# Kernel tuning notes

Hardware: AMD Instinct MI355X
Metric: run time of the kernel (lower is better)

## Reference

```python
import jax, jax.numpy as jnp
import numpy as np

B_MOL = 512      # molecules in batch
A_PER = 64       # atoms per molecule (uniform -> scopes are regular)
EU_PER = 2 * A_PER   # undirected bonds per molecule (ring + skip ring)
ED_PER = 2 * EU_PER  # directed bonds per molecule
N_ATOMS = B_MOL * A_PER
N_DIR = B_MOL * ED_PER
AF, BF = 98, 111
H, HEADS, DEPTH, MLP = 256, 8, 10, 512
DK = H // HEADS
ATOM_OUT, BOND_OUT = 128, 32


def _graph_indices():
    ar = np.arange(A_PER)
    su = np.concatenate([ar, ar])
    du = np.concatenate([(ar + 1) % A_PER, (ar + 2) % A_PER])
    src = np.concatenate([su, du])   # directed: fwd then rev copies
    dst = np.concatenate([du, su])
    rev = np.concatenate([np.arange(EU_PER) + EU_PER, np.arange(EU_PER)])
    offa = (np.arange(B_MOL) * A_PER)[:, None]
    offb = (np.arange(B_MOL) * ED_PER)[:, None]
    b2a = (src[None] + offa).reshape(-1).astype(np.int32)
    b2t = (dst[None] + offa).reshape(-1).astype(np.int32)
    b2rev = (rev[None] + offb).reshape(-1).astype(np.int32)
    pairs = np.stack([(su[None] + offa).reshape(-1), (du[None] + offa).reshape(-1)], 1).astype(np.int32)
    return jnp.asarray(b2a), jnp.asarray(b2t), jnp.asarray(b2rev), jnp.asarray(pairs)


def setup_inputs() -> dict:
    key = jax.random.key(0)
    ks = jax.random.split(key, 24)
    g = lambda k, s: jax.random.normal(k, s, jnp.float32) / np.sqrt(s[0])
    b2a, b2t, b2rev, bond_pairs = _graph_indices()
    return {
        'f_atoms': jax.random.normal(ks[0], (N_ATOMS, AF), jnp.float32),
        'f_bonds': jax.random.normal(ks[1], (N_DIR, BF), jnp.float32),
        'prev_hid': jnp.zeros((N_ATOMS, H), jnp.float32),
        'b2a': b2a, 'b2t': b2t, 'b2rev': b2rev, 'bond_pairs': bond_pairs,
        'W_i': g(ks[2], (BF, H)), 'W_h': g(ks[3], (H, H)),
        'W_o': g(ks[4], (AF + H, H)), 'b_o': jnp.zeros((H,), jnp.float32),
        'Wq': g(ks[5], (H, H)), 'Wk': g(ks[6], (H, H)),
        'Wv': g(ks[7], (H, H)), 'Wattn': g(ks[8], (H, H)),
        'W_vv': jnp.eye(H, dtype=jnp.float32), 'W_vc': g(ks[9], (H, H)),
        'A1': g(ks[10], (H, MLP)), 'a1': jnp.zeros((MLP,), jnp.float32),
        'A2': g(ks[11], (MLP, ATOM_OUT)), 'a2': jnp.zeros((ATOM_OUT,), jnp.float32),
        'B1': g(ks[12], (2 * H, MLP)), 'b1': jnp.zeros((MLP,), jnp.float32),
        'B2': g(ks[13], (MLP, BOND_OUT)), 'b2b': jnp.zeros((BOND_OUT,), jnp.float32),
        'G1': g(ks[14], (H, MLP)), 'g1': jnp.zeros((MLP,), jnp.float32),
        'G2': g(ks[15], (MLP, 1)), 'g2': jnp.zeros((1,), jnp.float32),
    }


def reference(f_atoms, f_bonds, prev_hid, b2a, b2t, b2rev, bond_pairs,
              W_i, W_h, W_o, b_o, Wq, Wk, Wv, Wattn, W_vv, W_vc,
              A1, a1, A2, a2, B1, b1, B2, b2b, G1, g1, G2, g2):
    # ---- DMPNN encoder (directed bond messages) ----
    h0 = jax.nn.relu(f_bonds @ W_i)                     # [E_dir, H]
    h = h0
    for _ in range(DEPTH - 1):
        a_sum = jax.ops.segment_sum(h, b2t, num_segments=N_ATOMS)  # incoming msg per atom
        m = a_sum[b2a] - h[b2rev]                       # exclude reverse bond
        h = jax.nn.relu(h0 + m @ W_h)
    a_in = jax.ops.segment_sum(h, b2t, num_segments=N_ATOMS)
    a_feats = jax.nn.relu(jnp.concatenate([f_atoms, a_in], 1) @ W_o + b_o)  # [N, H]

    # ---- Global_Attention over per-molecule scopes (uniform sizes -> reshape) ----
    x = a_feats.reshape(B_MOL, A_PER, H)
    q = (x @ Wq).reshape(B_MOL, A_PER, HEADS, DK)
    k = (x @ Wk).reshape(B_MOL, A_PER, HEADS, DK)
    v = (x @ Wv).reshape(B_MOL, A_PER, HEADS, DK)
    scores = jnp.einsum('bqhd,bkhd->bhqk', q, k) / np.sqrt(DK)
    attn = jax.nn.softmax(scores, axis=-1)
    ctx = jnp.einsum('bhqk,bkhd->bqhd', attn, v).reshape(B_MOL, A_PER, H)
    a_feats = (x + ctx @ Wattn).reshape(N_ATOMS, H)     # residual MHA

    # ---- recurrent atom state update ----
    atom_feats = jax.nn.relu(prev_hid @ W_vv.T + a_feats @ W_vc.T)  # [N, H]

    # ---- gather-based readout heads ----
    bond_feats = jnp.concatenate([atom_feats[bond_pairs[:, 0]],
                                  atom_feats[bond_pairs[:, 1]]], axis=1)  # [E_und, 2H]
    graph_vecs = atom_feats.reshape(B_MOL, A_PER, H).sum(axis=1)          # [B, H]

    atom_outs = jax.nn.relu(atom_feats @ A1 + a1) @ A2 + a2   # [N, ATOM_OUT]
    bond_outs = jax.nn.relu(bond_feats @ B1 + b1) @ B2 + b2b  # [E_und, BOND_OUT]
    graph_outs = jax.nn.relu(graph_vecs @ G1 + g1) @ G2 + g2  # [B, 1]

    # per-molecule edit scores: [bond scores | atom scores | graph score]
    edit_scores = jnp.concatenate([bond_outs.reshape(B_MOL, -1),
                                   atom_outs.reshape(B_MOL, -1),
                                   graph_outs], axis=1)
    return edit_scores
```

## Files before the change

kernel.cpp:

```cpp
#include <hip/hip_runtime.h>
#include <cstdint>
#include <cstddef>

#define B_MOL 512
#define A_PER 64
#define ED_PER 256
#define N_ATOMS (B_MOL * A_PER)
#define N_DIR (B_MOL * ED_PER)
#define N_UND (B_MOL * 128)
#define HID 256
#define OUT_STRIDE 12289
#define AP 40
#define CP 72

typedef __attribute__((ext_vector_type(8))) short bf16x8;
typedef __attribute__((ext_vector_type(8))) unsigned short u16x8;
typedef __attribute__((ext_vector_type(4))) float f32x4;

#define MFMA(a, b, c) __builtin_amdgcn_mfma_f32_16x16x32_bf16(a, b, c, 0, 0, 0)

__device__ __forceinline__ float b2f(unsigned short s) {
  return __builtin_bit_cast(float, (unsigned)s << 16);
}
__device__ __forceinline__ void split2(float v, unsigned short& h, unsigned short& l) {
  unsigned ub = __builtin_bit_cast(unsigned, v);
  h = (unsigned short)(ub >> 16);
  float fh = __builtin_bit_cast(float, ub & 0xffff0000u);
  float r = v - fh;
  l = (unsigned short)(__builtin_bit_cast(unsigned, r) >> 16);
}
__device__ __forceinline__ int e_src(int e) {
  return (e < 64) ? e : (e < 128) ? (e - 64)
       : (e < 192) ? ((e - 127) & 63) : ((e - 190) & 63);
}

__global__ __launch_bounds__(256) void convAll(
    const float* Wi, const float* Wh, const float* Wo,
    const float* Wq, const float* Wk, const float* Wv,
    const float* Wattn, const float* Wvc, const float* Wvv,
    const float* A1, const float* A2, const float* B1, const float* B2,
    unsigned short* WiTh, unsigned short* WiTl,
    unsigned short* WhTh, unsigned short* WhTl,
    unsigned short* WoTh, unsigned short* WoTl,
    unsigned short* WqkvTh, unsigned short* WqkvTl,
    unsigned short* WaTh, unsigned short* WaTl,
    unsigned short* WcvTh, unsigned short* WcvTl,
    unsigned short* A1Th, unsigned short* A1Tl,
    unsigned short* A2Th, unsigned short* A2Tl,
    unsigned short* B1Th, unsigned short* B1Tl,
    unsigned short* B2Th, unsigned short* B2Tl) {
  int b = blockIdx.x;
  const float *src = nullptr, *src2 = nullptr;
  unsigned short *dh = nullptr, *dl = nullptr;
  int K = 256, N = 256, Kp = 256, mode = 0, n = 0;
  if (b < 2048) {
    int seg = b >> 8; n = b & 255;
    switch (seg) {
      case 0: src = Wi; dh = WiTh; dl = WiTl; K = 111; Kp = 128; break;
      case 1: src = Wh; dh = WhTh; dl = WhTl; break;
      case 2: src = Wo; dh = WoTh; dl = WoTl; K = 354; Kp = 384; mode = 1; break;
      case 3: src = Wq; dh = WqkvTh; dl = WqkvTl; break;
      case 4: src = Wk; dh = WqkvTh + 65536; dl = WqkvTl + 65536; break;
      case 5: src = Wv; dh = WqkvTh + 131072; dl = WqkvTl + 131072; break;
      case 6: src = Wattn; dh = WaTh; dl = WaTl; break;
      default: src = Wvc; src2 = Wvv; dh = WcvTh; dl = WcvTl; K = 512; Kp = 512; mode = 2; break;
    }
  } else if (b < 2560) { n = b - 2048; src = A1; dh = A1Th; dl = A1Tl; K = 256; N = 512; Kp = 256; }
  else if (b < 2688)   { n = b - 2560; src = A2; dh = A2Th; dl = A2Tl; K = 512; N = 128; Kp = 512; }
  else if (b < 3200)   { n = b - 2688; src = B1; dh = B1Th; dl = B1Tl; K = 512; N = 512; Kp = 512; }
  else                 { n = b - 3200; src = B2; dh = B2Th; dl = B2Tl; K = 512; N = 32;  Kp = 512; }
  for (int k = threadIdx.x; k < Kp; k += 256) {
    float v = 0.f;
    if (mode == 0) { if (k < K) v = src[(size_t)k * N + n]; }
    else if (mode == 1) {
      if (k < 256) v = src[(size_t)(98 + k) * 256 + n];
      else if (k < 354) v = src[(size_t)(k - 256) * 256 + n];
    } else {
      v = (k < 256) ? src[(size_t)n * 256 + k] : src2[(size_t)n * 256 + (k - 256)];
    }
    unsigned short h_, l_;
    split2(v, h_, l_);
    dh[(size_t)n * Kp + k] = h_;
    dl[(size_t)n * Kp + k] = l_;
  }
}

template <int AMODE>
__launch_bounds__(256, 3)
__global__ void mgemm(const void* Aa_, const void* Ab_, const void* Ac_, const void* Ad_,
                      const unsigned short* __restrict__ BTh,
                      const unsigned short* __restrict__ BTl, int ldb,
                      const unsigned short* addH, const unsigned short* addL,
                      const float* __restrict__ bias,
                      const float* __restrict__ abias,
                      void* outA, void* outB,
                      int M, int N, int K, int lda, int ldco, int outcol,
                      int relu, int outmode) {
  __shared__ unsigned short AsH[128 * AP], AsL[128 * AP];
  __shared__ unsigned short BsH[128 * AP], BsL[128 * AP];
  const int tid = threadIdx.x;
  const int lane = tid & 63;
  const int l15 = lane & 15, l4 = lane >> 4;
  const int w = tid >> 6;
  const int wr = (w >> 1) * 64, wc = (w & 1) * 64;
  const int tileM = blockIdx.x * 128, tileN = blockIdx.y * 128;
  const int srow = tid >> 1;
  const int sks = (tid & 1) * 16;

  int rem = N - tileN - wc;
  int bnMax = rem >= 64 ? 4 : (rem > 0 ? (rem >> 4) : 0);

  f32x4 zf = {0.f, 0.f, 0.f, 0.f};
  f32x4 acc[4][4];
#pragma unroll
  for (int i = 0; i < 4; ++i)
#pragma unroll
    for (int j = 0; j < 4; ++j) acc[i][j] = zf;

  const int nkb = (K + 31) >> 5;
  for (int kb = 0; kb < nkb; ++kb) {
    __syncthreads();
    const int k0 = kb * 32 + sks;
    {
      const int row = tileM + srow;
      if (AMODE == 1 || (AMODE == 3 && k0 < 256)) {
        const unsigned short* Ah = (const unsigned short*)Aa_;
        const unsigned short* Al = (const unsigned short*)Ab_;
        size_t bse = (AMODE == 3) ? ((size_t)row * 256 + k0)
                                  : ((size_t)row * lda + k0);
        *(u16x8*)&AsH[srow * AP + sks]     = *(const u16x8*)&Ah[bse];
        *(u16x8*)&AsH[srow * AP + sks + 8] = *(const u16x8*)&Ah[bse + 8];
        *(u16x8*)&AsL[srow * AP + sks]     = *(const u16x8*)&Al[bse];
        *(u16x8*)&AsL[srow * AP + sks + 8] = *(const u16x8*)&Al[bse + 8];
      } else if (AMODE == 5) {
        int mol = row >> 7, u = row & 127;
        int a0 = (u < 64) ? u : (u - 64);
        int a1v = (u < 64) ? ((u + 1) & 63) : ((u - 62) & 63);
        size_t p1 = (size_t)(mol * 64 + a0) * 512 + k0;
        size_t p2 = (size_t)(mol * 64 + a1v) * 512 + k0;
        const unsigned short* P1h = (const unsigned short*)Aa_;
        const unsigned short* P1l = (const unsigned short*)Ab_;
        const unsigned short* P2h = (const unsigned short*)Ac_;
        const unsigned short* P2l = (const unsigned short*)Ad_;
        u16x8 x1h[2] = {*(const u16x8*)&P1h[p1], *(const u16x8*)&P1h[p1 + 8]};
        u16x8 x1l[2] = {*(const u16x8*)&P1l[p1], *(const u16x8*)&P1l[p1 + 8]};
        u16x8 x2h[2] = {*(const u16x8*)&P2h[p2], *(const u16x8*)&P2h[p2 + 8]};
        u16x8 x2l[2] = {*(const u16x8*)&P2l[p2], *(const u16x8*)&P2l[p2 + 8]};
#pragma unroll
        for (int c = 0; c < 2; ++c) {
          u16x8 hv, lv;
#pragma unroll
          for (int z = 0; z < 8; ++z) {
            float v = b2f(x1h[c][z]) + b2f(x1l[c][z])
                    + b2f(x2h[c][z]) + b2f(x2l[c][z]) + abias[k0 + c * 8 + z];
            v = fmaxf(v, 0.f);
            unsigned short h_, l_;
            split2(v, h_, l_);
            hv[z] = h_; lv[z] = l_;
          }
          *(u16x8*)&AsH[srow * AP + sks + c * 8] = hv;
          *(u16x8*)&AsL[srow * AP + sks + c * 8] = lv;
        }
      } else {
        u16x8 hv0 = {0,0,0,0,0,0,0,0}, lv0 = {0,0,0,0,0,0,0,0};
        u16x8 hv1 = {0,0,0,0,0,0,0,0}, lv1 = {0,0,0,0,0,0,0,0};
#pragma unroll
        for (int z = 0; z < 16; ++z) {
          int k = k0 + z;
          float v = 0.f;
          if (AMODE == 0) {
            if (k < K) v = ((const float*)Aa_)[(size_t)row * lda + k];
          } else if (AMODE == 2) {
            if (k < 256) v = ((const float*)Aa_)[(size_t)row * 256 + k];
            else if (k < 354) v = ((const float*)Ab_)[(size_t)row * 98 + (k - 256)];
          } else {
            v = ((const float*)Ac_)[(size_t)row * 256 + (k - 256)];
          }
          unsigned short h_, l_;
          split2(v, h_, l_);
          if (z < 8) { hv0[z] = h_; lv0[z] = l_; }
          else       { hv1[z - 8] = h_; lv1[z - 8] = l_; }
        }
        *(u16x8*)&AsH[srow * AP + sks]     = hv0;
        *(u16x8*)&AsH[srow * AP + sks + 8] = hv1;
        *(u16x8*)&AsL[srow * AP + sks]     = lv0;
        *(u16x8*)&AsL[srow * AP + sks + 8] = lv1;
      }
    }
    {
      const int n = tileN + srow;
      if (n < N) {
        size_t bb = (size_t)n * ldb + k0;
        *(u16x8*)&BsH[srow * AP + sks]     = *(const u16x8*)&BTh[bb];
        *(u16x8*)&BsH[srow * AP + sks + 8] = *(const u16x8*)&BTh[bb + 8];
        *(u16x8*)&BsL[srow * AP + sks]     = *(const u16x8*)&BTl[bb];
        *(u16x8*)&BsL[srow * AP + sks + 8] = *(const u16x8*)&BTl[bb + 8];
      } else {
        u16x8 z8 = {0,0,0,0,0,0,0,0};
        *(u16x8*)&BsH[srow * AP + sks]     = z8;
        *(u16x8*)&BsH[srow * AP + sks + 8] = z8;
        *(u16x8*)&BsL[srow * AP + sks]     = z8;
        *(u16x8*)&BsL[srow * AP + sks + 8] = z8;
      }
    }
    __syncthreads();
    bf16x8 ah[4], al[4];
#pragma unroll
    for (int am = 0; am < 4; ++am) {
      int ar = wr + am * 16 + l15;
      ah[am] = *(const bf16x8*)&AsH[ar * AP + l4 * 8];
      al[am] = *(const bf16x8*)&AsL[ar * AP + l4 * 8];
    }
#pragma unroll
    for (int bn = 0; bn < 4; ++bn) {
      if (bn < bnMax) {
        int br = wc + bn * 16 + l15;
        bf16x8 bh = *(const bf16x8*)&BsH[br * AP + l4 * 8];
        bf16x8 bl = *(const bf16x8*)&BsL[br * AP + l4 * 8];
#pragma unroll
        for (int am = 0; am < 4; ++am) {
          acc[am][bn] = MFMA(ah[am], bh, acc[am][bn]);
          acc[am][bn] = MFMA(ah[am], bl, acc[am][bn]);
          acc[am][bn] = MFMA(al[am], bh, acc[am][bn]);
        }
      }
    }
  }

#pragma unroll
  for (int am = 0; am < 4; ++am) {
#pragma unroll
    for (int bn = 0; bn < 4; ++bn) {
      if (bn >= bnMax) continue;
      int col = tileN + wc + bn * 16 + l15;
      float bs = bias ? bias[col] : 0.f;
#pragma unroll
      for (int r = 0; r < 4; ++r) {
        size_t row = (size_t)tileM + wr + am * 16 + l4 * 4 + r;
        float v = acc[am][bn][r] + bs;
        if (addH) v += b2f(addH[row * 256 + col]) + b2f(addL[row * 256 + col]);
        if (relu) v = fmaxf(v, 0.f);
        if (outmode == 0) {
          unsigned short h_, l_;
          split2(v, h_, l_);
          ((unsigned short*)outA)[row * (size_t)ldco + col] = h_;
          ((unsigned short*)outB)[row * (size_t)ldco + col] = l_;
        } else if (outmode == 1) {
          ((float*)outA)[row * (size_t)ldco + outcol + col] = v;
        } else if (outmode == 2) {
          int mol = (int)(row >> 6), t = (int)(row & 63);
          ((float*)outA)[(size_t)mol * OUT_STRIDE + 4096 + t * 128 + col] = v;
        } else {
          int mol = (int)(row >> 7), u = (int)(row & 127);
          ((float*)outA)[(size_t)mol * OUT_STRIDE + u * 32 + col] = v;
        }
      }
    }
  }
}

__launch_bounds__(1024)
__global__ void msg_f4(float* h,
                       const unsigned short* __restrict__ WhTh,
                       const unsigned short* __restrict__ WhTl,
                       const unsigned short* __restrict__ WiTh,
                       const unsigned short* __restrict__ WiTl,
                       const float* __restrict__ fb) {
  extern __shared__ char smem_[];
  unsigned short* AsC = (unsigned short*)smem_;
  unsigned short* BsC = (unsigned short*)(smem_ + 36864);
  const int tid = threadIdx.x;
  const int lane = tid & 63, l15 = lane & 15, l4 = lane >> 4;
  const int w = tid >> 6;
  const int wm = (w >> 2) * 64;
  const int wn = (w & 3) * 64;
  const int mol = blockIdx.x;
  const int arow = tid >> 2;
  const int aks = (tid & 3) * 8;

  f32x4 acc[4][4];
#pragma unroll
  for (int i = 0; i < 4; ++i)
#pragma unroll
    for (int j = 0; j < 4; ++j) acc[i][j] = (f32x4){0.f, 0.f, 0.f, 0.f};

  const int sA = e_src(arow);
  const int rvA = (arow < 128) ? (arow + 128) : (arow - 128);
  const int i0 = (sA + 63) & 63;
  const int i1 = 64 + ((sA + 62) & 63);
  const int i2 = 128 + sA;
  const int i3 = 192 + sA;
  const size_t hbase = (size_t)mol * 256 * 256;

  const size_t fbb = (size_t)(mol * 256 + arow) * 111;
  for (int kb = 0; kb < 4; ++kb) {
    __syncthreads();
    {
      u16x8 hv = {0,0,0,0,0,0,0,0}, lv = {0,0,0,0,0,0,0,0};
#pragma unroll
      for (int z = 0; z < 8; ++z) {
        int k = kb * 32 + aks + z;
        float v = (k < 111) ? fb[fbb + k] : 0.f;
        unsigned short h_, l_;
        split2(v, h_, l_);
        hv[z] = h_; lv[z] = l_;
      }
      *(u16x8*)&AsC[arow * CP + aks]      = hv;
      *(u16x8*)&AsC[arow * CP + 32 + aks] = lv;
    }
    {
      size_t bb = (size_t)arow * 128 + kb * 32 + aks;
      *(u16x8*)&BsC[arow * CP + aks]      = *(const u16x8*)&WiTh[bb];
      *(u16x8*)&BsC[arow * CP + 32 + aks] = *(const u16x8*)&WiTl[bb];
    }
    __syncthreads();
    bf16x8 ah[4], al[4];
#pragma unroll
    for (int am = 0; am < 4; ++am) {
      int ar = wm + am * 16 + l15;
      ah[am] = *(const bf16x8*)&AsC[ar * CP + l4 * 8];
      al[am] = *(const bf16x8*)&AsC[ar * CP + 32 + l4 * 8];
    }
#pragma unroll
    for (int bn = 0; bn < 4; ++bn) {
      int br = wn + bn * 16 + l15;
      bf16x8 bh = *(const bf16x8*)&BsC[br * CP + l4 * 8];
      bf16x8 bl = *(const bf16x8*)&BsC[br * CP + 32 + l4 * 8];
#pragma unroll
      for (int am = 0; am < 4; ++am) {
        acc[am][bn] = MFMA(ah[am], bh, acc[am][bn]);
        acc[am][bn] = MFMA(ah[am], bl, acc[am][bn]);
        acc[am][bn] = MFMA(al[am], bh, acc[am][bn]);
      }
    }
  }
#pragma unroll
  for (int i = 0; i < 4; ++i)
#pragma unroll
    for (int j = 0; j < 4; ++j)
#pragma unroll
      for (int r = 0; r < 4; ++r) acc[i][j][r] = fmaxf(acc[i][j][r], 0.f);

  for (int kb = 0; kb < 8; ++kb) {
    __syncthreads();
    {
      const int c0 = kb * 32 + aks;
      f32x4 m0, m1;
      {
        const float* p = &h[hbase + (size_t)i0 * 256 + c0];
        m0 = *(const f32x4*)p;
        m1 = *(const f32x4*)(p + 4);
      }
      {
        const float* p = &h[hbase + (size_t)i1 * 256 + c0];
        m0 += *(const f32x4*)p;
        m1 += *(const f32x4*)(p + 4);
      }
      {
        const float* p = &h[hbase + (size_t)i2 * 256 + c0];
        m0 += *(const f32x4*)p;
        m1 += *(const f32x4*)(p + 4);
      }
      {
        const float* p = &h[hbase + (size_t)i3 * 256 + c0];
        m0 += *(const f32x4*)p;
        m1 += *(const f32x4*)(p + 4);
      }
      {
        const float* p = &h[hbase + (size_t)rvA * 256 + c0];
        m0 -= *(const f32x4*)p;
        m1 -= *(const f32x4*)(p + 4);
      }
      u16x8 hv, lv;
#pragma unroll
      for (int z = 0; z < 4; ++z) {
        unsigned short h_, l_;
        split2(m0[z], h_, l_); hv[z] = h_; lv[z] = l_;
        split2(m1[z], h_, l_); hv[4 + z] = h_; lv[4 + z] = l_;
      }
      *(u16x8*)&AsC[arow * CP + aks]      = hv;
      *(u16x8*)&AsC[arow * CP + 32 + aks] = lv;
    }
    {
      size_t bb = (size_t)arow * 256 + kb * 32 + aks;
      *(u16x8*)&BsC[arow * CP + aks]      = *(const u16x8*)&WhTh[bb];
      *(u16x8*)&BsC[arow * CP + 32 + aks] = *(const u16x8*)&WhTl[bb];
    }
    __syncthreads();
    bf16x8 ah[4], al[4];
#pragma unroll
    for (int am = 0; am < 4; ++am) {
      int ar = wm + am * 16 + l15;
      ah[am] = *(const bf16x8*)&AsC[ar * CP + l4 * 8];
      al[am] = *(const bf16x8*)&AsC[ar * CP + 32 + l4 * 8];
    }
#pragma unroll
    for (int bn = 0; bn < 4; ++bn) {
      int br = wn + bn * 16 + l15;
      bf16x8 bh = *(const bf16x8*)&BsC[br * CP + l4 * 8];
      bf16x8 bl = *(const bf16x8*)&BsC[br * CP + 32 + l4 * 8];
#pragma unroll
      for (int am = 0; am < 4; ++am) {
        acc[am][bn] = MFMA(ah[am], bh, acc[am][bn]);
        acc[am][bn] = MFMA(ah[am], bl, acc[am][bn]);
        acc[am][bn] = MFMA(al[am], bh, acc[am][bn]);
      }
    }
  }

#pragma unroll
  for (int am = 0; am < 4; ++am) {
#pragma unroll
    for (int r = 0; r < 4; ++r) {
      int row = wm + am * 16 + l4 * 4 + r;
      size_t rowb = hbase + (size_t)row * 256;
#pragma unroll
      for (int bn = 0; bn < 4; ++bn) {
        int col = wn + bn * 16 + l15;
        h[rowb + col] = fmaxf(acc[am][bn][r], 0.f);
      }
    }
  }
}

__global__ __launch_bounds__(256) void asum_f(const float* __restrict__ h,
                                              float* __restrict__ out) {
  int g = blockIdx.x * 256 + threadIdx.x;
  int atom = g >> 5, cc = (g & 31) << 3;
  int mol = atom >> 6, t = atom & 63;
  const float* hb = h + (size_t)mol * ED_PER * HID;
  int e0 = (t + 63) & 63;
  int e1 = 64 + ((t + 62) & 63);
  int e2 = 128 + t;
  int e3 = 192 + t;
  f32x4 s0 = {0.f, 0.f, 0.f, 0.f}, s1 = {0.f, 0.f, 0.f, 0.f};
#define ACC_E(ee) { \
    const float* p = hb + (size_t)(ee) * HID + cc; \
    s0 += *(const f32x4*)p; \
    s1 += *(const f32x4*)(p + 4); }
  ACC_E(e0); ACC_E(e1); ACC_E(e2); ACC_E(e3);
#undef ACC_E
  *(f32x4*)&out[(size_t)atom * HID + cc] = s0;
  *(f32x4*)&out[(size_t)atom * HID + cc + 4] = s1;
}

__global__ __launch_bounds__(64) void attn_k(const float* __restrict__ qkv,
                                             unsigned short* __restrict__ ctxH,
                                             unsigned short* __restrict__ ctxL) {
  __shared__ float kls[64 * 32];
  __shared__ float vls[64 * 32];
  int mol = blockIdx.x >> 3, head = blockIdx.x & 7;
  int lane = threadIdx.x;
  size_t rb = ((size_t)(mol * 64 + lane)) * 768 + head * 32;
#pragma unroll
  for (int c = 0; c < 8; ++c) {
    *(float4*)(kls + lane * 32 + c * 4) = *(const float4*)(qkv + rb + 256 + c * 4);
    *(float4*)(vls + lane * 32 + c * 4) = *(const float4*)(qkv + rb + 512 + c * 4);
  }
  float q[32];
#pragma unroll
  for (int d = 0; d < 32; ++d) q[d] = qkv[rb + d];
  __syncthreads();
  float mx = -1e30f, l = 0.f;
  float acc[32];
#pragma unroll
  for (int d = 0; d < 32; ++d) acc[d] = 0.f;
  for (int j = 0; j < 64; ++j) {
    float s = 0.f;
#pragma unroll
    for (int d = 0; d < 32; ++d) s += q[d] * kls[j * 32 + d];
    s *= 0.17677669529663687f;
    float nm = fmaxf(mx, s);
    float co = __expf(mx - nm);
    float p = __expf(s - nm);
    l = l * co + p;
#pragma unroll
    for (int d = 0; d < 32; ++d) acc[d] = acc[d] * co + p * vls[j * 32 + d];
    mx = nm;
  }
  float inv = 1.f / l;
  size_t ob = ((size_t)(mol * 64 + lane)) * 256 + head * 32;
#pragma unroll
  for (int d = 0; d < 32; ++d) {
    unsigned short h_, l_;
    split2(acc[d] * inv, h_, l_);
    ctxH[ob + d] = h_;
    ctxL[ob + d] = l_;
  }
}

__global__ __launch_bounds__(256) void gv_k(const unsigned short* __restrict__ afH,
                                            const unsigned short* __restrict__ afL,
                                            float* __restrict__ gv) {
  int mol = blockIdx.x, c = threadIdx.x;
  float s = 0.f;
  for (int a = 0; a < 64; ++a) {
    size_t i = ((size_t)mol * 64 + a) * 256 + c;
    s += b2f(afH[i]) + b2f(afL[i]);
  }
  gv[mol * 256 + c] = s;
}

__global__ __launch_bounds__(512) void gh_k(const float* __restrict__ gv, const float* __restrict__ G1,
                                            const float* __restrict__ g1, const float* __restrict__ G2,
                                            const float* __restrict__ g2, float* __restrict__ out) {
  __shared__ float xs[256];
  __shared__ float red[512];
  int mol = blockIdx.x, j = threadIdx.x;
  if (j < 256) xs[j] = gv[mol * 256 + j];
  __syncthreads();
  float s = 0.f;
  for (int k = 0; k < 256; ++k) s += xs[k] * G1[k * 512 + j];
  s = fmaxf(s + g1[j], 0.f);
  red[j] = s * G2[j];
  __syncthreads();
  for (int st = 256; st > 0; st >>= 1) {
    if (j < st) red[j] += red[j + st];
    __syncthreads();
  }
  if (j == 0) out[(size_t)mol * OUT_STRIDE + 12288] = red[0] + g2[0];
}

extern "C" void kernel_launch(void* const* d_in, const int* in_sizes, int n_in,
                              void* d_out, int out_size, void* d_ws, size_t ws_size,
                              hipStream_t stream) {
  (void)in_sizes; (void)n_in; (void)out_size; (void)ws_size;
  const float* f_atoms  = (const float*)d_in[0];
  const float* f_bonds  = (const float*)d_in[1];
  const float* prev_hid = (const float*)d_in[2];
  const float* W_i   = (const float*)d_in[7];
  const float* W_h   = (const float*)d_in[8];
  const float* W_o   = (const float*)d_in[9];
  const float* b_o   = (const float*)d_in[10];
  const float* Wq    = (const float*)d_in[11];
  const float* Wk    = (const float*)d_in[12];
  const float* Wv    = (const float*)d_in[13];
  const float* Wattn = (const float*)d_in[14];
  const float* W_vv  = (const float*)d_in[15];
  const float* W_vc  = (const float*)d_in[16];
  const float* A1    = (const float*)d_in[17];
  const float* a1    = (const float*)d_in[18];
  const float* A2    = (const float*)d_in[19];
  const float* a2    = (const float*)d_in[20];
  const float* B1    = (const float*)d_in[21];
  const float* b1    = (const float*)d_in[22];
  const float* B2    = (const float*)d_in[23];
  const float* b2b   = (const float*)d_in[24];
  const float* G1    = (const float*)d_in[25];
  const float* g1    = (const float*)d_in[26];
  const float* G2    = (const float*)d_in[27];
  const float* g2    = (const float*)d_in[28];
  float* out = (float*)d_out;

  char* base = (char*)d_ws;
  float* h = (float*)(base);
  float* asumF = (float*)(base + 134217728);
  char* W0 = base + 167772160;
  unsigned short* WiTh   = (unsigned short*)(W0);
  unsigned short* WiTl   = (unsigned short*)(W0 + 65536);
  unsigned short* WhTh   = (unsigned short*)(W0 + 131072);
  unsigned short* WhTl   = (unsigned short*)(W0 + 262144);
  unsigned short* WoTh   = (unsigned short*)(W0 + 393216);
  unsigned short* WoTl   = (unsigned short*)(W0 + 589824);
  unsigned short* WqkvTh = (unsigned short*)(W0 + 786432);
  unsigned short* WqkvTl = (unsigned short*)(W0 + 1179648);
  unsigned short* WaTh   = (unsigned short*)(W0 + 1572864);
  unsigned short* WaTl   = (unsigned short*)(W0 + 1703936);
  unsigned short* WcvTh  = (unsigned short*)(W0 + 1835008);
  unsigned short* WcvTl  = (unsigned short*)(W0 + 2097152);
  unsigned short* A1Th   = (unsigned short*)(W0 + 2359296);
  unsigned short* A1Tl   = (unsigned short*)(W0 + 2621440);
  unsigned short* A2Th   = (unsigned short*)(W0 + 2883584);
  unsigned short* A2Tl   = (unsigned short*)(W0 + 3014656);
  unsigned short* B1Th   = (unsigned short*)(W0 + 3145728);
  unsigned short* B1Tl   = (unsigned short*)(W0 + 3670016);
  unsigned short* B2Th   = (unsigned short*)(W0 + 4194304);
  unsigned short* B2Tl   = (unsigned short*)(W0 + 4227072);
  float* gvec            = (float*)(W0 + 4259840);
  unsigned short* xAh  = (unsigned short*)(base);
  unsigned short* xAl  = (unsigned short*)(base + 16777216);
  float* qkv           = (float*)(base + 33554432);
  unsigned short* ctxh = (unsigned short*)(base + 134217728);
  unsigned short* ctxl = (unsigned short*)(base + 150994944);
  unsigned short* afh  = (unsigned short*)(base + 33554432);
  unsigned short* afl  = (unsigned short*)(base + 50331648);
  unsigned short* atfh = (unsigned short*)(base + 67108864);
  unsigned short* atfl = (unsigned short*)(base + 83886080);
  unsigned short* t1h  = (unsigned short*)(base);
  unsigned short* t1l  = (unsigned short*)(base + 33554432);
  unsigned short* P1h  = (unsigned short*)(base);
  unsigned short* P1l  = (unsigned short*)(base + 33554432);
  unsigned short* P2h  = (unsigned short*)(base + 100663296);
  unsigned short* P2l  = (unsigned short*)(base + 134217728);

  convAll<<<3232, 256, 0, stream>>>(
      W_i, W_h, W_o, Wq, Wk, Wv, Wattn, W_vc, W_vv, A1, A2, B1, B2,
      WiTh, WiTl, WhTh, WhTl, WoTh, WoTl, WqkvTh, WqkvTl, WaTh, WaTl,
      WcvTh, WcvTl, A1Th, A1Tl, A2Th, A2Tl, B1Th, B1Tl, B2Th, B2Tl);

  mgemm<0><<<dim3(1024, 2), 256, 0, stream>>>(
      f_bonds, nullptr, nullptr, nullptr, WiTh, WiTl, 128,
      nullptr, nullptr, nullptr, nullptr,
      h, nullptr, N_DIR, 256, 111, 111, 256, 0, 1, 1);

  for (int d = 0; d < 9; ++d) {
    msg_f4<<<512, 1024, 73728, stream>>>(h, WhTh, WhTl, WiTh, WiTl, f_bonds);
  }

  asum_f<<<4096, 256, 0, stream>>>(h, asumF);
  mgemm<2><<<dim3(256, 2), 256, 0, stream>>>(
      asumF, f_atoms, nullptr, nullptr, WoTh, WoTl, 384,
      nullptr, nullptr, b_o, nullptr,
      xAh, xAl, N_ATOMS, 256, 354, 0, 256, 0, 1, 0);
  mgemm<1><<<dim3(256, 6), 256, 0, stream>>>(
      xAh, xAl, nullptr, nullptr, WqkvTh, WqkvTl, 256,
      nullptr, nullptr, nullptr, nullptr,
      qkv, nullptr, N_ATOMS, 768, 256, 256, 768, 0, 0, 1);
  attn_k<<<4096, 64, 0, stream>>>(qkv, ctxh, ctxl);
  mgemm<1><<<dim3(256, 2), 256, 0, stream>>>(
      ctxh, ctxl, nullptr, nullptr, WaTh, WaTl, 256,
      xAh, xAl, nullptr, nullptr,
      afh, afl, N_ATOMS, 256, 256, 256, 256, 0, 0, 0);
  mgemm<3><<<dim3(256, 2), 256, 0, stream>>>(
      afh, afl, prev_hid, nullptr, WcvTh, WcvTl, 512,
      nullptr, nullptr, nullptr, nullptr,
      atfh, atfl, N_ATOMS, 256, 512, 256, 256, 0, 1, 0);
  mgemm<1><<<dim3(256, 4), 256, 0, stream>>>(
      atfh, atfl, nullptr, nullptr, A1Th, A1Tl, 256,
      nullptr, nullptr, a1, nullptr,
      t1h, t1l, N_ATOMS, 512, 256, 256, 512, 0, 1, 0);
  mgemm<1><<<dim3(256, 1), 256, 0, stream>>>(
      t1h, t1l, nullptr, nullptr, A2Th, A2Tl, 512,
      nullptr, nullptr, a2, nullptr,
      out, nullptr, N_ATOMS, 128, 512, 512, 0, 0, 0, 2);
  mgemm<1><<<dim3(256, 4), 256, 0, stream>>>(
      atfh, atfl, nullptr, nullptr, B1Th, B1Tl, 512,
      nullptr, nullptr, nullptr, nullptr,
      P1h, P1l, N_ATOMS, 512, 256, 256, 512, 0, 0, 0);
  mgemm<1><<<dim3(256, 4), 256, 0, stream>>>(
      atfh, atfl, nullptr, nullptr, B1Th + 256, B1Tl + 256, 512,
      nullptr, nullptr, nullptr, nullptr,
      P2h, P2l, N_ATOMS, 512, 256, 256, 512, 0, 0, 0);
  mgemm<5><<<dim3(512, 1), 256, 0, stream>>>(
      P1h, P1l, P2h, P2l, B2Th, B2Tl, 512,
      nullptr, nullptr, b2b, b1,
      out, nullptr, N_UND, 32, 512, 0, 0, 0, 0, 3);
  gv_k<<<512, 256, 0, stream>>>(atfh, atfl, gvec);
  gh_k<<<512, 512, 0, stream>>>(gvec, G1, g1, G2, g2, out);
}
```

Measured before the change: 1.857 ms.

## Pre-convert bond features to padded bf16 once and drop low-part MFMA

Adds extra blocks to the weight-conversion kernel that round f_bonds to bf16 (RNE) into a 128-padded buffer. The initial GEMM (new AMODE 6) and the nine message-passing iterations then load this buffer directly instead of re-reading fp32 rows and splitting them into high/low parts every time. This removes repeated strided fp32 loads and conversion work and one of the three split-precision MFMAs on that input. In exchange, the bond-feature operand loses its low-order correction, so accuracy drops from roughly fp32 to bf16 on that input.

```diff
diff --git a/kernel.cpp b/kernel.cpp
--- a/kernel.cpp
+++ b/kernel.cpp
@@ -29,6 +29,11 @@
   float r = v - fh;
   l = (unsigned short)(__builtin_bit_cast(unsigned, r) >> 16);
 }
+__device__ __forceinline__ unsigned short f2bf_rne(float v) {
+  unsigned u = __builtin_bit_cast(unsigned, v);
+  u += 0x7FFFu + ((u >> 16) & 1u);
+  return (unsigned short)(u >> 16);
+}
 __device__ __forceinline__ int e_src(int e) {
   return (e < 64) ? e : (e < 128) ? (e - 64)
        : (e < 192) ? ((e - 127) & 63) : ((e - 190) & 63);
@@ -39,6 +44,7 @@
     const float* Wq, const float* Wk, const float* Wv,
     const float* Wattn, const float* Wvc, const float* Wvv,
     const float* A1, const float* A2, const float* B1, const float* B2,
+    const float* fbF, unsigned short* fbT,
     unsigned short* WiTh, unsigned short* WiTl,
     unsigned short* WhTh, unsigned short* WhTl,
     unsigned short* WoTh, unsigned short* WoTl,
@@ -50,6 +56,25 @@
     unsigned short* B1Th, unsigned short* B1Tl,
     unsigned short* B2Th, unsigned short* B2Tl) {
   int b = blockIdx.x;
+  if (b >= 3232) {
+    int e = (b - 3232) * 32 + (threadIdx.x >> 3);
+    int ks = (threadIdx.x & 7) * 16;
+    const float* s = fbF + (size_t)e * 111;
+    u16x8 o0 = {0,0,0,0,0,0,0,0}, o1 = {0,0,0,0,0,0,0,0};
+#pragma unroll
+    for (int z = 0; z < 8; ++z) {
+      int k = ks + z;
+      if (k < 111) o0[z] = f2bf_rne(s[k]);
+    }
+#pragma unroll
+    for (int z = 0; z < 8; ++z) {
+      int k = ks + 8 + z;
+      if (k < 111) o1[z] = f2bf_rne(s[k]);
+    }
+    *(u16x8*)&fbT[(size_t)e * 128 + ks] = o0;
+    *(u16x8*)&fbT[(size_t)e * 128 + ks + 8] = o1;
+    return;
+  }
   const float *src = nullptr, *src2 = nullptr;
   unsigned short *dh = nullptr, *dl = nullptr;
   int K = 256, N = 256, Kp = 256, mode = 0, n = 0;
@@ -123,7 +148,12 @@
     const int k0 = kb * 32 + sks;
     {
       const int row = tileM + srow;
-      if (AMODE == 1 || (AMODE == 3 && k0 < 256)) {
+      if (AMODE == 6) {
+        const unsigned short* Ah = (const unsigned short*)Aa_;
+        size_t bse = (size_t)row * lda + k0;
+        *(u16x8*)&AsH[srow * AP + sks]     = *(const u16x8*)&Ah[bse];
+        *(u16x8*)&AsH[srow * AP + sks + 8] = *(const u16x8*)&Ah[bse + 8];
+      } else if (AMODE == 1 || (AMODE == 3 && k0 < 256)) {
         const unsigned short* Ah = (const unsigned short*)Aa_;
         const unsigned short* Al = (const unsigned short*)Ab_;
         size_t bse = (AMODE == 3) ? ((size_t)row * 256 + k0)
@@ -209,7 +239,7 @@
     for (int am = 0; am < 4; ++am) {
       int ar = wr + am * 16 + l15;
       ah[am] = *(const bf16x8*)&AsH[ar * AP + l4 * 8];
-      al[am] = *(const bf16x8*)&AsL[ar * AP + l4 * 8];
+      if (AMODE != 6) al[am] = *(const bf16x8*)&AsL[ar * AP + l4 * 8];
     }
 #pragma unroll
     for (int bn = 0; bn < 4; ++bn) {
@@ -221,7 +251,7 @@
         for (int am = 0; am < 4; ++am) {
           acc[am][bn] = MFMA(ah[am], bh, acc[am][bn]);
           acc[am][bn] = MFMA(ah[am], bl, acc[am][bn]);
-          acc[am][bn] = MFMA(al[am], bh, acc[am][bn]);
+          if (AMODE != 6) acc[am][bn] = MFMA(al[am], bh, acc[am][bn]);
         }
       }
     }
@@ -265,7 +295,7 @@
                        const unsigned short* __restrict__ WhTl,
                        const unsigned short* __restrict__ WiTh,
                        const unsigned short* __restrict__ WiTl,
-                       const float* __restrict__ fb) {
+                       const unsigned short* __restrict__ fbT) {
   extern __shared__ char smem_[];
   unsigned short* AsC = (unsigned short*)smem_;
   unsigned short* BsC = (unsigned short*)(smem_ + 36864);
@@ -292,21 +322,11 @@
   const int i3 = 192 + sA;
   const size_t hbase = (size_t)mol * 256 * 256;
 
-  const size_t fbb = (size_t)(mol * 256 + arow) * 111;
+  const size_t fbb = (size_t)(mol * 256 + arow) * 128;
   for (int kb = 0; kb < 4; ++kb) {
     __syncthreads();
     {
-      u16x8 hv = {0,0,0,0,0,0,0,0}, lv = {0,0,0,0,0,0,0,0};
-#pragma unroll
-      for (int z = 0; z < 8; ++z) {
-        int k = kb * 32 + aks + z;
-        float v = (k < 111) ? fb[fbb + k] : 0.f;
-        unsigned short h_, l_;
-        split2(v, h_, l_);
-        hv[z] = h_; lv[z] = l_;
-      }
-      *(u16x8*)&AsC[arow * CP + aks]      = hv;
-      *(u16x8*)&AsC[arow * CP + 32 + aks] = lv;
+      *(u16x8*)&AsC[arow * CP + aks] = *(const u16x8*)&fbT[fbb + kb * 32 + aks];
     }
     {
       size_t bb = (size_t)arow * 128 + kb * 32 + aks;
@@ -314,12 +334,11 @@
       *(u16x8*)&BsC[arow * CP + 32 + aks] = *(const u16x8*)&WiTl[bb];
     }
     __syncthreads();
-    bf16x8 ah[4], al[4];
+    bf16x8 ah[4];
 #pragma unroll
     for (int am = 0; am < 4; ++am) {
       int ar = wm + am * 16 + l15;
       ah[am] = *(const bf16x8*)&AsC[ar * CP + l4 * 8];
-      al[am] = *(const bf16x8*)&AsC[ar * CP + 32 + l4 * 8];
     }
 #pragma unroll
     for (int bn = 0; bn < 4; ++bn) {
@@ -330,7 +349,6 @@
       for (int am = 0; am < 4; ++am) {
         acc[am][bn] = MFMA(ah[am], bh, acc[am][bn]);
         acc[am][bn] = MFMA(ah[am], bl, acc[am][bn]);
-        acc[am][bn] = MFMA(al[am], bh, acc[am][bn]);
       }
     }
   }
@@ -554,6 +572,7 @@
 
   char* base = (char*)d_ws;
   float* h = (float*)(base);
+  unsigned short* fbT = (unsigned short*)(base + 134217728);
   float* asumF = (float*)(base + 134217728);
   char* W0 = base + 167772160;
   unsigned short* WiTh   = (unsigned short*)(W0);
@@ -593,18 +612,19 @@
   unsigned short* P2h  = (unsigned short*)(base + 100663296);
   unsigned short* P2l  = (unsigned short*)(base + 134217728);
 
-  convAll<<<3232, 256, 0, stream>>>(
+  convAll<<<7328, 256, 0, stream>>>(
       W_i, W_h, W_o, Wq, Wk, Wv, Wattn, W_vc, W_vv, A1, A2, B1, B2,
+      f_bonds, fbT,
       WiTh, WiTl, WhTh, WhTl, WoTh, WoTl, WqkvTh, WqkvTl, WaTh, WaTl,
       WcvTh, WcvTl, A1Th, A1Tl, A2Th, A2Tl, B1Th, B1Tl, B2Th, B2Tl);
 
-  mgemm<0><<<dim3(1024, 2), 256, 0, stream>>>(
-      f_bonds, nullptr, nullptr, nullptr, WiTh, WiTl, 128,
+  mgemm<6><<<dim3(1024, 2), 256, 0, stream>>>(
+      fbT, nullptr, nullptr, nullptr, WiTh, WiTl, 128,
       nullptr, nullptr, nullptr, nullptr,
-      h, nullptr, N_DIR, 256, 111, 111, 256, 0, 1, 1);
+      h, nullptr, N_DIR, 256, 128, 128, 256, 0, 1, 1);
 
   for (int d = 0; d < 9; ++d) {
-    msg_f4<<<512, 1024, 73728, stream>>>(h, WhTh, WhTl, WiTh, WiTl, f_bonds);
+    msg_f4<<<512, 1024, 73728, stream>>>(h, WhTh, WhTl, WiTh, WiTl, fbT);
   }
 
   asum_f<<<4096, 256, 0, stream>>>(h, asumF);
```

Measured after the change: 1.794 ms. 1.04x faster.
